# Kernel optimization log

Hardware: AMD Instinct MI355X
Metric: run time of the kernel (lower is better)

## Reference

```python
import jax, jax.numpy as jnp
import numpy as np

# Module constants (from init_kwargs)
NB_IN = 4          # num_blocks_in
NB_OUT = 8         # num_blocks_out
BS_IN = 128        # block_size_in (hard-coded in source)
NHID = 4096
BS_OUT = NHID // NB_OUT   # 512, also att_out
TOPK = 4
DK = 64            # d_k = d_v, n_head = 1


def _group_linear(x, w):
    # x: (B, n_blocks, d_in), w: (n_blocks, d_in, d_out) -> (B, n_blocks, d_out)
    return jnp.einsum('bnd,nde->bne', x, w)


def _attend(q, k, v):
    # single-head scaled dot-product attention
    attn = jax.nn.softmax(jnp.einsum('bqd,bkd->bqk', q, k) / jnp.sqrt(jnp.asarray(DK, q.dtype)), axis=-1)
    return jnp.einsum('bqk,bkd->bqd', attn, v), attn


def setup_inputs() -> dict:
    key = jax.random.key(0)
    ks = jax.random.split(key, 20)
    s = 0.02
    d = {
        'inp': jax.random.normal(ks[0], (1024, NB_IN * BS_IN), jnp.float32),
        'hx': jax.random.normal(ks[1], (1024, NHID), jnp.float32),
        'cx': jax.random.normal(ks[2], (1024, NHID), jnp.float32),
        # inp_att (residual=False): GroupLinear q/k/v + fc
        'ia_wq': jax.random.normal(ks[3], (NB_OUT, BS_OUT, DK), jnp.float32) * s,
        'ia_wk': jax.random.normal(ks[4], (NB_IN + 1, BS_IN, DK), jnp.float32) * s,
        'ia_wv': jax.random.normal(ks[5], (NB_IN + 1, BS_IN, DK), jnp.float32) * s,
        'ia_fc_w': jax.random.normal(ks[6], (DK, BS_OUT), jnp.float32) * s,
        'ia_fc_b': jnp.zeros((BS_OUT,), jnp.float32),
        # mha (residual=True, gated)
        'mha_wq': jax.random.normal(ks[7], (NB_OUT, BS_OUT, DK), jnp.float32) * s,
        'mha_wk': jax.random.normal(ks[8], (NB_OUT, BS_OUT, DK), jnp.float32) * s,
        'mha_wv': jax.random.normal(ks[9], (NB_OUT, BS_OUT, DK), jnp.float32) * s,
        'mha_fc_w': jax.random.normal(ks[10], (DK, BS_OUT), jnp.float32) * s,
        'mha_fc_b': jnp.zeros((BS_OUT,), jnp.float32),
        'mha_gate_w': jax.random.normal(ks[11], (DK, BS_OUT), jnp.float32) * s,
        'mha_gate_b': jnp.zeros((BS_OUT,), jnp.float32),
        # block-diagonal LSTM (BlockLSTM after blockify_params): per-block LSTMCell
        'w_ih': jax.random.normal(ks[12], (NB_OUT, BS_OUT, 4 * BS_OUT), jnp.float32) * s,
        'w_hh': jax.random.normal(ks[13], (NB_OUT, BS_OUT, 4 * BS_OUT), jnp.float32) * s,
        'b_ih': jnp.zeros((NB_OUT, 4 * BS_OUT), jnp.float32),
        'b_hh': jnp.zeros((NB_OUT, 4 * BS_OUT), jnp.float32),
    }
    return d


def _forward(inp, hx, cx, ia_wq, ia_wk, ia_wv, ia_fc_w, ia_fc_b,
             mha_wq, mha_wk, mha_wv, mha_fc_w, mha_fc_b, mha_gate_w, mha_gate_b,
             w_ih, w_hh, b_ih, b_hh):
    B = inp.shape[0]
    # --- input attention (inp_att) ---
    x = inp.reshape(B, NB_IN, BS_IN)
    x = jnp.concatenate([x, jnp.zeros_like(x[:, :1])], axis=1)        # append null block -> (B, NB_IN+1, BS_IN)
    hb = hx.reshape(B, NB_OUT, BS_OUT)
    q = _group_linear(hb, ia_wq)                                      # (B, NB_OUT, DK)
    k = _group_linear(x, ia_wk)
    v = _group_linear(x, ia_wv)
    o, iatt = _attend(q, k, v)                                        # o:(B,NB_OUT,DK), iatt:(B,NB_OUT,NB_IN+1)
    inp_use = (o @ ia_fc_w + ia_fc_b).reshape(B, NB_OUT * BS_OUT)     # residual=False path

    # --- top-k block selection mask (detached) ---
    score = iatt[:, :, 0]                                             # (B, NB_OUT)
    thr = jax.lax.top_k(score, TOPK)[0][:, -1]                        # k-th largest per sample
    mask_blk = (score > thr[:, None] - 0.01).astype(hx.dtype)         # (B, NB_OUT)
    mask = jnp.broadcast_to(mask_blk[:, :, None], (B, NB_OUT, BS_OUT)).reshape(B, NHID)
    mask = jax.lax.stop_gradient(mask)

    # --- block-diagonal LSTM update ---
    xb = inp_use.reshape(B, NB_OUT, BS_OUT)
    cb = cx.reshape(B, NB_OUT, BS_OUT)
    gates = (jnp.einsum('bkd,kdg->bkg', xb, w_ih) + b_ih
             + jnp.einsum('bkd,kdg->bkg', hb, w_hh) + b_hh)           # (B, NB_OUT, 4*BS_OUT)
    i_g, f_g, g_g, o_g = jnp.split(gates, 4, axis=-1)
    c_new = jax.nn.sigmoid(f_g) * cb + jax.nn.sigmoid(i_g) * jnp.tanh(g_g)
    h_new = jax.nn.sigmoid(o_g) * jnp.tanh(c_new)                     # (B, NB_OUT, BS_OUT)
    cx_new = c_new.reshape(B, NHID)

    # --- inter-block attention (step_att, residual + gate) ---
    residual = h_new
    q2 = _group_linear(h_new, mha_wq)
    k2 = _group_linear(h_new, mha_wk)
    v2 = _group_linear(h_new, mha_wv)
    o2, _ = _attend(q2, k2, v2)                                       # (B, NB_OUT, DK)
    out = o2 @ mha_fc_w + mha_fc_b
    gate = jax.nn.sigmoid(o2 @ mha_gate_w + mha_gate_b)
    hx_new = (residual + gate * jnp.tanh(out)).reshape(B, NHID)

    # --- masked blend of old / new states ---
    hx_out = mask * hx_new + (1.0 - mask) * hx
    cx_out = mask * cx_new + (1.0 - mask) * cx
    return hx_out, cx_out, mask


def reference(inp, hx, cx, ia_wq, ia_wk, ia_wv, ia_fc_w, ia_fc_b,
              mha_wq, mha_wk, mha_wv, mha_fc_w, mha_fc_b, mha_gate_w, mha_gate_b,
              w_ih, w_hh, b_ih, b_hh):
    return _forward(inp, hx, cx, ia_wq, ia_wk, ia_wv, ia_fc_w, ia_fc_b,
                    mha_wq, mha_wk, mha_wv, mha_fc_w, mha_fc_b, mha_gate_w, mha_gate_b,
                    w_ih, w_hh, b_ih, b_hh)
```

## Files before the change

kernel.cpp:

```cpp
#include <hip/hip_runtime.h>
#include <hip/hip_bf16.h>

#define B_    1024
#define NHID_ 4096
#define NBO   8
#define BSO   512
#define DK_   64

typedef __bf16 bf16;
typedef __bf16 bf16x2 __attribute__((ext_vector_type(2)));
typedef __bf16 bf16x4 __attribute__((ext_vector_type(4)));
typedef __bf16 bf16x8 __attribute__((ext_vector_type(8)));
typedef float  f32x4  __attribute__((ext_vector_type(4)));

__device__ __forceinline__ float sigf(float x){
    float e = __expf(-x);
    return __builtin_amdgcn_rcpf(1.0f + e);
}
__device__ __forceinline__ float ftanh(float x){
    float e = __expf(2.0f*x);
    return 1.0f - 2.0f*__builtin_amdgcn_rcpf(e + 1.0f);
}

__device__ __forceinline__ void gload16(const void* g, void* lds){
    __builtin_amdgcn_global_load_lds((const __attribute__((address_space(1))) unsigned int*)g,
                                     (__attribute__((address_space(3))) unsigned int*)lds,
                                     16, 0, 0);
}

__device__ __forceinline__ void sbar(){
    asm volatile("" ::: "memory");
    __builtin_amdgcn_s_barrier();
    asm volatile("" ::: "memory");
}
#define WAITVM(N) asm volatile("s_waitcnt vmcnt(" #N ")" ::: "memory")

__global__ __launch_bounds__(256) void k_prepqkv(
    const float* __restrict__ w_ih, const float* __restrict__ w_hh,
    const float* __restrict__ hx, const float* __restrict__ inp,
    const float* __restrict__ ia_wq, const float* __restrict__ ia_wk,
    const float* __restrict__ ia_wv,
    const float* __restrict__ mha_wq, const float* __restrict__ mha_wk,
    const float* __restrict__ mha_wv, const float* __restrict__ ia_fc_w,
    const float* __restrict__ fc_w, const float* __restrict__ gate_w,
    bf16* __restrict__ wT, bf16* __restrict__ hb16, bf16* __restrict__ wqkvT,
    bf16* __restrict__ iafcT, bf16* __restrict__ fcgT,
    float* __restrict__ qbufH, float* __restrict__ kbufH, float* __restrict__ vbufH)
{
    int bid = blockIdx.x;
    int t = threadIdx.x;
    __shared__ float Af[32][36];
    __shared__ float W1[32][68];
    __shared__ float W2[32][68];
    __shared__ float tile[64][65];

    if (bid < 768){
        int z = (bid >= 384) ? 1 : 0;
        int r = bid - z*384;
        int y = r >> 5, b0 = (r & 31)*32;
        int tx = t&15, ty = t>>4;
        if (y < 8){
            int n = y;
            float acc[2][4] = {};
            for (int k0=z*256; k0<z*256+256; k0+=32){
                { int row=t>>3, c4=(t&7)*4;
                  *(float4*)&Af[row][c4] = *(const float4*)&hx[(size_t)(b0+row)*4096 + n*512 + k0 + c4]; }
                #pragma unroll
                for (int j=0;j<2;++j){
                    int id = j*256 + t;
                    int kk = id>>4, e4 = (id&15)*4;
                    *(float4*)&W1[kk][e4] = *(const float4*)&ia_wq[(size_t)n*32768 + (size_t)(k0+kk)*64 + e4];
                }
                __syncthreads();
                #pragma unroll
                for (int kk4=0; kk4<8; ++kk4){
                    float4 a0 = *(float4*)&Af[ty*2  ][kk4*4];
                    float4 a1 = *(float4*)&Af[ty*2+1][kk4*4];
                    #pragma unroll
                    for (int j=0;j<4;++j){
                        float4 wv = *(float4*)&W1[kk4*4+j][tx*4];
                        float s0 = (j==0)?a0.x:((j==1)?a0.y:((j==2)?a0.z:a0.w));
                        float s1 = (j==0)?a1.x:((j==1)?a1.y:((j==2)?a1.z:a1.w));
                        acc[0][0]+=s0*wv.x; acc[0][1]+=s0*wv.y; acc[0][2]+=s0*wv.z; acc[0][3]+=s0*wv.w;
                        acc[1][0]+=s1*wv.x; acc[1][1]+=s1*wv.y; acc[1][2]+=s1*wv.z; acc[1][3]+=s1*wv.w;
                    }
                }
                __syncthreads();
            }
            #pragma unroll
            for (int r2=0;r2<2;++r2){
                float4 o; o.x=acc[r2][0]; o.y=acc[r2][1]; o.z=acc[r2][2]; o.w=acc[r2][3];
                *(float4*)&qbufH[((size_t)(z*B_ + b0+ty*2+r2))*512 + n*64 + tx*4] = o;
            }
        } else {
            int jb = y-8;
            float ak[2][4] = {}, av[2][4] = {};
            for (int k0=z*64; k0<z*64+64; k0+=32){
                { int row=t>>3, c4=(t&7)*4;
                  *(float4*)&Af[row][c4] = *(const float4*)&inp[(size_t)(b0+row)*512 + jb*128 + k0 + c4]; }
                #pragma unroll
                for (int j=0;j<2;++j){
                    int id = j*256 + t;
                    int kk = id>>4, e4 = (id&15)*4;
                    *(float4*)&W1[kk][e4] = *(const float4*)&ia_wk[(size_t)jb*8192 + (size_t)(k0+kk)*64 + e4];
                    *(float4*)&W2[kk][e4] = *(const float4*)&ia_wv[(size_t)jb*8192 + (size_t)(k0+kk)*64 + e4];
                }
                __syncthreads();
                #pragma unroll
                for (int kk4=0; kk4<8; ++kk4){
                    float4 a0 = *(float4*)&Af[ty*2  ][kk4*4];
                    float4 a1 = *(float4*)&Af[ty*2+1][kk4*4];
                    #pragma unroll
                    for (int j=0;j<4;++j){
                        float4 wk = *(float4*)&W1[kk4*4+j][tx*4];
                        float4 wv = *(float4*)&W2[kk4*4+j][tx*4];
                        float s0 = (j==0)?a0.x:((j==1)?a0.y:((j==2)?a0.z:a0.w));
                        float s1 = (j==0)?a1.x:((j==1)?a1.y:((j==2)?a1.z:a1.w));
                        ak[0][0]+=s0*wk.x; ak[0][1]+=s0*wk.y; ak[0][2]+=s0*wk.z; ak[0][3]+=s0*wk.w;
                        ak[1][0]+=s1*wk.x; ak[1][1]+=s1*wk.y; ak[1][2]+=s1*wk.z; ak[1][3]+=s1*wk.w;
                        av[0][0]+=s0*wv.x; av[0][1]+=s0*wv.y; av[0][2]+=s0*wv.z; av[0][3]+=s0*wv.w;
                        av[1][0]+=s1*wv.x; av[1][1]+=s1*wv.y; av[1][2]+=s1*wv.z; av[1][3]+=s1*wv.w;
                    }
                }
                __syncthreads();
            }
            #pragma unroll
            for (int r2=0;r2<2;++r2){
                float4 ok; ok.x=ak[r2][0]; ok.y=ak[r2][1]; ok.z=ak[r2][2]; ok.w=ak[r2][3];
                float4 ov; ov.x=av[r2][0]; ov.y=av[r2][1]; ov.z=av[r2][2]; ov.w=av[r2][3];
                *(float4*)&kbufH[((size_t)(z*B_ + b0+ty*2+r2))*256 + jb*64 + tx*4] = ok;
                *(float4*)&vbufH[((size_t)(z*B_ + b0+ty*2+r2))*256 + jb*64 + tx*4] = ov;
            }
        }
        return;
    }
    bid -= 768;
    if (bid < 4096){
        int c0 = (bid & 31)*64;
        int k0 = ((bid>>5)&7)*64;
        int z  = bid>>8;
        int n = z>>1, which = z&1;
        const float* src = (which ? w_hh : w_ih) + (size_t)n*512*2048;
        #pragma unroll
        for (int it=0; it<4; ++it){
            int idx = t + it*256;
            int r = idx>>4, c4 = (idx&15)*4;
            *(float4*)&tile[r][c4] = *(const float4*)&src[(size_t)(k0+r)*2048 + c0 + c4];
        }
        __syncthreads();
        #pragma unroll
        for (int it=0; it<2; ++it){
            int idx = t + it*256;
            int c = idx>>3, r8 = (idx&7)*8;
            bf16x8 v;
            #pragma unroll
            for (int jj=0;jj<8;++jj) v[jj] = (bf16)tile[r8+jj][c];
            *(bf16x8*)&wT[((size_t)n*2048 + c0 + c)*1024 + which*512 + k0 + r8] = v;
        }
        return;
    }
    int gid = (bid-4096)*256 + t;
    if (gid < 1048576){
        float4 v = ((const float4*)hx)[gid];
        bf16x4 o; o.x=(bf16)v.x; o.y=(bf16)v.y; o.z=(bf16)v.z; o.w=(bf16)v.w;
        *(bf16x4*)&hb16[(size_t)gid*4] = o;
        return;
    }
    int e = gid - 1048576;
    if (e < 786432){
        int col = e >> 9, k = e & 511;
        int n = col / 192, c = col - n*192;
        int p = c >> 6, ee = c & 63;
        const float* s = (p==0) ? mha_wq : ((p==1) ? mha_wk : mha_wv);
        wqkvT[e] = (bf16)s[((size_t)n*512 + k)*64 + ee];
        return;
    }
    e -= 786432;
    if (e < 32768){
        int c = e>>6, k = e&63;
        iafcT[e] = (bf16)ia_fc_w[(size_t)k*512 + c];
        return;
    }
    e -= 32768;
    if (e < 65536){
        int cg = e>>6, k = e&63;
        int ct = cg>>6, j = cg&63;
        const float* s = (j<32) ? fc_w : gate_w;
        int col = ct*32 + (j&31);
        fcgT[e] = (bf16)s[(size_t)k*512 + col];
    }
}

__global__ __launch_bounds__(512) void k_score(const float* __restrict__ qbufH,
                                               const float* __restrict__ kbufH,
                                               const float* __restrict__ vbufH,
                                               const bf16* __restrict__ iafcT,
                                               const float* __restrict__ ia_fc_b,
                                               bf16* __restrict__ xb16,
                                               float* __restrict__ maskb,
                                               float* __restrict__ mask_out)
{
    int t = threadIdx.x;
    int sb = t>>7, ts = t&127;
    int wv = (t>>6)&1, lw = t&63;
    int b = blockIdx.x*4 + sb;
    __shared__ float q_s[4][512];
    __shared__ float k_s[4][256];
    __shared__ float v_s[4][256];
    __shared__ float at_s[4][40];
    __shared__ float sc_s[4][8];
    __shared__ float mb_s[4][8];
    __shared__ bf16 o_s[32][72];

    #pragma unroll
    for (int r=0;r<4;++r){
        int i = ts + r*128;
        q_s[sb][i] = qbufH[(size_t)b*512 + i] + qbufH[(size_t)(B_+b)*512 + i];
    }
    #pragma unroll
    for (int r=0;r<2;++r){
        int i = ts + r*128;
        k_s[sb][i] = kbufH[(size_t)b*256 + i] + kbufH[(size_t)(B_+b)*256 + i];
        v_s[sb][i] = vbufH[(size_t)b*256 + i] + vbufH[(size_t)(B_+b)*256 + i];
    }
    __syncthreads();
    {
        int n = wv*4 + (lw>>4);
        int j = (lw>>2)&3;
        int ec = lw&3;
        const float* q = &q_s[sb][n*64 + ec*16];
        const float* k = &k_s[sb][j*64 + ec*16];
        float s = 0.f;
        #pragma unroll
        for (int e=0;e<16;++e) s += q[e]*k[e];
        s += __shfl_xor(s, 1);
        s += __shfl_xor(s, 2);
        if (ec==0) at_s[sb][n*5+j] = s*0.125f;
        if ((lw&15)==4) at_s[sb][n*5+4] = 0.f;
    }
    __syncthreads();
    if (lw < 4){
        int n = wv*4 + lw;
        float m = at_s[sb][n*5];
        for (int j=1;j<5;++j) m = fmaxf(m, at_s[sb][n*5+j]);
        float ex[5]; float sum=0.f;
        for (int j=0;j<5;++j){ ex[j]=__expf(at_s[sb][n*5+j]-m); sum+=ex[j]; }
        float inv = 1.f/sum;
        for (int j=0;j<5;++j) at_s[sb][n*5+j] = ex[j]*inv;
        sc_s[sb][n] = ex[0]*inv;
    }
    __syncthreads();
    if (ts == 0){
        float s[8];
        for (int nn=0;nn<8;++nn) s[nn] = sc_s[sb][nn];
        for (int ii=1;ii<8;++ii){ float key=s[ii]; int jj=ii-1;
            while(jj>=0 && s[jj]<key){ s[jj+1]=s[jj]; --jj; } s[jj+1]=key; }
        float thr = s[3]-0.01f;
        for (int nn=0;nn<8;++nn) mb_s[sb][nn] = (sc_s[sb][nn] > thr) ? 1.0f : 0.0f;
    }
    __syncthreads();
    #pragma unroll
    for (int r=0;r<4;++r){
        int i = ts + r*128;
        int n = i>>6, e = i&63;
        float s = 0.f;
        #pragma unroll
        for (int j=0;j<4;++j) s += at_s[sb][n*5+j]*v_s[sb][j*64+e];
        o_s[sb*8+n][e] = (bf16)s;
    }
    if (ts < 8) maskb[b*8+ts] = mb_s[sb][ts];
    float4* mo = (float4*)(mask_out + (size_t)b*4096);
    #pragma unroll
    for (int r=0;r<8;++r){
        int i4 = ts + r*128;
        float m = mb_s[sb][i4>>7];
        float4 mv; mv.x=m; mv.y=m; mv.z=m; mv.w=m;
        mo[i4] = mv;
    }
    __syncthreads();
    {
        int w = t>>6, l = t&63, quad = l>>4, l16 = l&15;
        int wm = w&1, wd = w>>1;
        bf16x8 a0 = *(const bf16x8*)&o_s[wm*16 + l16][quad*8];
        bf16x8 a1 = *(const bf16x8*)&o_s[wm*16 + l16][32 + quad*8];
        f32x4 zero = {0.f,0.f,0.f,0.f};
        #pragma unroll
        for (int nt=0; nt<8; ++nt){
            int cg = wd*128 + nt*16 + l16;
            bf16x8 b0 = *(const bf16x8*)&iafcT[(size_t)cg*64 + quad*8];
            bf16x8 b1 = *(const bf16x8*)&iafcT[(size_t)cg*64 + 32 + quad*8];
            f32x4 acc = __builtin_amdgcn_mfma_f32_16x16x32_bf16(a0, b0, zero, 0,0,0);
            acc = __builtin_amdgcn_mfma_f32_16x16x32_bf16(a1, b1, acc, 0,0,0);
            float bias = ia_fc_b[cg];
            #pragma unroll
            for (int v=0; v<4; ++v){
                int rm = wm*16 + quad*4 + v;
                int bb = blockIdx.x*4 + (rm>>3), nn = rm&7;
                xb16[(size_t)bb*4096 + nn*512 + cg] = (bf16)(acc[v] + bias);
            }
        }
    }
}

__global__ __launch_bounds__(512,2) void k_lstm(
    const bf16* __restrict__ xb16, const bf16* __restrict__ hb16,
    const bf16* __restrict__ wT, const float* __restrict__ b_ih,
    const float* __restrict__ b_hh, const float* __restrict__ cx,
    const float* __restrict__ maskb,
    float* __restrict__ cx_out, bf16* __restrict__ hn16)
{
    int bid = blockIdx.x;
    int n  = bid & 7;
    int i  = bid >> 3;
    int mt = i & 3, nt = i >> 2;
    int b0 = mt*256, d0 = nt*64;

    int t = threadIdx.x;
    int w = t >> 6, l = t & 63;
    int wr = w >> 2, wc = w & 3;
    int quad = l >> 4, l16 = l & 15;

    __shared__ __align__(16) bf16 lds[4*16384];

    int G0 = t;
    int rowA0 = G0>>2, rowA1 = rowA0 + 128;
    int ksA0 = (G0&3) ^ ((rowA0>>1)&3);
    int ksA1 = (G0&3) ^ ((rowA1>>1)&3);
    const bf16* xbP0 = xb16 + (size_t)(b0+rowA0)*4096 + n*512 + ksA0*8;
    const bf16* hbP0 = hb16 + (size_t)(b0+rowA0)*4096 + n*512 + ksA0*8;
    const bf16* xbP1 = xb16 + (size_t)(b0+rowA1)*4096 + n*512 + ksA1*8;
    const bf16* hbP1 = hb16 + (size_t)(b0+rowA1)*4096 + n*512 + ksA1*8;

    int vc0 = G0>>2, vc1 = vc0 + 128;
    int ksB0 = (G0&3) ^ ((vc0>>1)&3);
    int ksB1 = (G0&3) ^ ((vc1>>1)&3);
    const bf16* wb = wT + (size_t)n*2048*1024;
    const bf16* wP0 = wb + (size_t)((vc0>>6)*512 + d0 + (vc0&63))*1024 + ksB0*8;
    const bf16* wP1 = wb + (size_t)((vc1>>6)*512 + d0 + (vc1&63))*1024 + ksB1*8;

    int offA[8], offB[4];
    #pragma unroll
    for (int m=0;m<8;++m){ int R = wr*128 + m*16 + l16; offA[m] = (R*4 + (quad ^ ((R>>1)&3)))*8; }
    #pragma unroll
    for (int nf=0;nf<4;++nf){ int C = wc*64 + nf*16 + l16; offB[nf] = (C*4 + (quad ^ ((C>>1)&3)))*8; }

    auto stA = [&](int buf, int kt){
        const bf16* s0 = (kt<16 ? xbP0 : hbP0) + (kt&15)*32;
        const bf16* s1 = (kt<16 ? xbP1 : hbP1) + (kt&15)*32;
        bf16* dst = &lds[buf*16384 + w*512];
        gload16(s0, dst);
        gload16(s1, dst + 4096);
    };
    auto stB = [&](int buf, int kt){
        bf16* dst = &lds[buf*16384 + 8192 + w*512];
        gload16(wP0 + kt*32, dst);
        gload16(wP1 + kt*32, dst + 4096);
    };

    f32x4 zero = {0.f,0.f,0.f,0.f};
    f32x4 acc[8][4];
    #pragma unroll
    for (int m=0;m<8;++m)
        #pragma unroll
        for (int nf=0;nf<4;++nf) acc[m][nf] = zero;

    stA(0,0); stB(0,0);
    stA(1,1); stB(1,1);
    WAITVM(4);
    sbar();

    #pragma unroll 2
    for (int kt=0; kt<32; ++kt){
        int buf = kt & 3;
        const bf16* Ab = &lds[buf*16384];
        const bf16* Bb = Ab + 8192;

        if (kt < 30){ stA((kt+2)&3, kt+2); stB((kt+2)&3, kt+2); }

        bf16x8 av[8], bv[4];
        #pragma unroll
        for (int m=0;m<8;++m) av[m] = *(const bf16x8*)&Ab[offA[m]];
        #pragma unroll
        for (int nf=0;nf<4;++nf) bv[nf] = *(const bf16x8*)&Bb[offB[nf]];

        __builtin_amdgcn_s_setprio(1);
        #pragma unroll
        for (int m=0;m<8;++m)
            #pragma unroll
            for (int nf=0;nf<4;++nf)
                acc[m][nf] = __builtin_amdgcn_mfma_f32_16x16x32_bf16(av[m], bv[nf], acc[m][nf], 0,0,0);
        __builtin_amdgcn_s_setprio(0);

        if (kt < 30) { WAITVM(4); } else { WAITVM(0); }
        sbar();
    }

    float* gbuf = (float*)lds;
    const int GP = 260;
    int dl_t = t & 63;
    int i_t  = t >> 6;
    int d = d0 + dl_t;
    float bi  = b_ih[n*2048 +        d] + b_hh[n*2048 +        d];
    float bff = b_ih[n*2048 +  512 + d] + b_hh[n*2048 +  512 + d];
    float bg  = b_ih[n*2048 + 1024 + d] + b_hh[n*2048 + 1024 + d];
    float bo  = b_ih[n*2048 + 1536 + d] + b_hh[n*2048 + 1536 + d];

    #pragma unroll
    for (int c=0; c<4; ++c){
        if (wr == (c>>1)){
            #pragma unroll
            for (int mm=0; mm<4; ++mm)
                #pragma unroll
                for (int nf=0; nf<4; ++nf)
                    #pragma unroll
                    for (int v=0; v<4; ++v)
                        gbuf[(mm*16 + quad*4 + v)*GP + wc*64 + nf*16 + l16] = acc[(c&1)*4 + mm][nf][v];
        }
        __syncthreads();
        #pragma unroll
        for (int r=0; r<8; ++r){
            int row_l = i_t*8 + r;
            int row_g = b0 + c*64 + row_l;
            float gi = gbuf[row_l*GP +       dl_t] + bi;
            float gf = gbuf[row_l*GP +  64 + dl_t] + bff;
            float gg = gbuf[row_l*GP + 128 + dl_t] + bg;
            float go = gbuf[row_l*GP + 192 + dl_t] + bo;
            size_t gidx = (size_t)row_g*4096 + n*512 + d;
            float cb = cx[gidx];
            float cn = sigf(gf)*cb + sigf(gi)*ftanh(gg);
            float hn = sigf(go)*ftanh(cn);
            float mk = maskb[row_g*8 + n];
            cx_out[gidx] = (mk != 0.f) ? cn : cb;
            hn16[gidx]   = (bf16)hn;
        }
        __syncthreads();
    }
}

__global__ __launch_bounds__(256) void k_proj64(const bf16* __restrict__ hn16,
                                                const bf16* __restrict__ wqkvT,
                                                float* __restrict__ qkv2)
{
    int b0 = blockIdx.x*64, n = blockIdx.y, ct = blockIdx.z;
    int t = threadIdx.x, w = t>>6, l = t&63, quad = l>>4, l16 = l&15;
    int wm = w&1, wd = w>>1;
    __shared__ bf16 A_s[2][256*8];
    __shared__ bf16 B_s[2][256*8];
    f32x4 zero = {0.f,0.f,0.f,0.f};
    f32x4 acc[2][2] = {{zero,zero},{zero,zero}};
    const bf16* ab = hn16 + (size_t)n*512;
    const bf16* wb = wqkvT + ((size_t)n*192 + ct*64)*512;

    auto stage = [&](int buf, int k0){
        int row = t>>2, ss = t&3;
        int seg = ss ^ ((row>>1)&3);
        gload16(ab + (size_t)(b0+row)*4096 + k0 + seg*8, &A_s[buf][(w*64)*8]);
        gload16(wb + (size_t)row*512      + k0 + seg*8, &B_s[buf][(w*64)*8]);
    };

    stage(0, 0);
    for (int it=0; it<16; ++it){
        __syncthreads();
        if (it < 15) stage((it+1)&1, (it+1)*32);
        int buf = it&1;
        bf16x8 a[2], bb[2];
        #pragma unroll
        for (int r=0;r<2;++r){
            int row = wm*32 + r*16 + l16;
            int slot = row*4 + (quad ^ ((row>>1)&3));
            a[r] = *(const bf16x8*)&A_s[buf][slot*8];
        }
        #pragma unroll
        for (int c=0;c<2;++c){
            int col = wd*32 + c*16 + l16;
            int slot = col*4 + (quad ^ ((col>>1)&3));
            bb[c] = *(const bf16x8*)&B_s[buf][slot*8];
        }
        #pragma unroll
        for (int r=0;r<2;++r)
            #pragma unroll
            for (int c=0;c<2;++c)
                acc[r][c] = __builtin_amdgcn_mfma_f32_16x16x32_bf16(a[r], bb[c], acc[r][c], 0,0,0);
    }
    #pragma unroll
    for (int c=0;c<2;++c){
        int col = ct*64 + wd*32 + c*16 + l16;
        #pragma unroll
        for (int r=0;r<2;++r)
            #pragma unroll
            for (int v=0;v<4;++v){
                int row = b0 + wm*32 + r*16 + quad*4 + v;
                qkv2[(size_t)row*1536 + n*192 + col] = acc[r][c][v];
            }
    }
}

__global__ __launch_bounds__(512) void k_att2fc(const float* __restrict__ qkv2,
                                                const bf16* __restrict__ fcgT,
                                                const float* __restrict__ fc_b,
                                                const float* __restrict__ gate_b,
                                                const bf16* __restrict__ hn16,
                                                const float* __restrict__ hx,
                                                const float* __restrict__ maskb,
                                                float* __restrict__ hx_out)
{
    int t = threadIdx.x;
    int sb = t>>7, ts = t&127;
    int wv = (t>>6)&1, lw = t&63;
    int b = blockIdx.x*4 + sb;
    __shared__ float q_s[4][512];
    __shared__ float k_s[4][512];
    __shared__ float v_s[4][512];
    __shared__ float at_s[4][64];
    __shared__ bf16 o_s[32][72];
    #pragma unroll
    for (int r=0;r<4;++r){
        int i = ts + r*128;
        int n = i>>6, e = i&63;
        const float* src = qkv2 + (size_t)b*1536 + n*192;
        q_s[sb][i] = src[e];
        k_s[sb][i] = src[64+e];
        v_s[sb][i] = src[128+e];
    }
    __syncthreads();
    {
        int n = wv*4 + (lw>>4);
        int j = (lw>>1)&7;
        int eh = lw&1;
        const float* q = &q_s[sb][n*64 + eh*32];
        const float* k = &k_s[sb][j*64 + eh*32];
        float s = 0.f;
        #pragma unroll
        for (int e=0;e<32;++e) s += q[e]*k[e];
        s += __shfl_xor(s, 1);
        if (eh==0) at_s[sb][n*8+j] = s*0.125f;
    }
    __syncthreads();
    if (lw < 4){
        int n = wv*4 + lw;
        float m = at_s[sb][n*8];
        for (int j=1;j<8;++j) m = fmaxf(m, at_s[sb][n*8+j]);
        float ex[8]; float sum=0.f;
        for (int j=0;j<8;++j){ ex[j]=__expf(at_s[sb][n*8+j]-m); sum+=ex[j]; }
        float inv = 1.f/sum;
        for (int j=0;j<8;++j) at_s[sb][n*8+j] = ex[j]*inv;
    }
    __syncthreads();
    #pragma unroll
    for (int r=0;r<4;++r){
        int i = ts + r*128;
        int n = i>>6, e = i&63;
        float s = 0.f;
        #pragma unroll
        for (int j=0;j<8;++j) s += at_s[sb][n*8+j]*v_s[sb][j*64+e];
        o_s[sb*8+n][e] = (bf16)s;
    }
    __syncthreads();
    {
        int w = t>>6, l = t&63, quad = l>>4, l16 = l&15;
        int wm = w&1, wd = w>>1;
        bf16x8 a0 = *(const bf16x8*)&o_s[wm*16 + l16][quad*8];
        bf16x8 a1 = *(const bf16x8*)&o_s[wm*16 + l16][32 + quad*8];
        f32x4 zero = {0.f,0.f,0.f,0.f};
        f32x4 acc[16];
        #pragma unroll
        for (int nt=0; nt<16; ++nt){
            int cg = wd*256 + nt*16 + l16;
            bf16x8 b0 = *(const bf16x8*)&fcgT[(size_t)cg*64 + quad*8];
            bf16x8 b1 = *(const bf16x8*)&fcgT[(size_t)cg*64 + 32 + quad*8];
            acc[nt] = __builtin_amdgcn_mfma_f32_16x16x32_bf16(a0, b0, zero, 0,0,0);
            acc[nt] = __builtin_amdgcn_mfma_f32_16x16x32_bf16(a1, b1, acc[nt], 0,0,0);
        }
        #pragma unroll
        for (int ctl=0; ctl<4; ++ctl){
            int ct = wd*4 + ctl;
            #pragma unroll
            for (int s=0; s<2; ++s){
                int d = ct*32 + s*16 + l16;
                float fb = fc_b[d], gb = gate_b[d];
                f32x4 fa = acc[ctl*4+s], ga = acc[ctl*4+2+s];
                #pragma unroll
                for (int v=0; v<4; ++v){
                    int rm = wm*16 + quad*4 + v;
                    int bb = blockIdx.x*4 + (rm>>3), nn = rm&7;
                    size_t idx = (size_t)bb*4096 + nn*512 + d;
                    float f = fa[v] + fb;
                    float g = ga[v] + gb;
                    float hnv = (float)hn16[idx];
                    float mk = maskb[bb*8+nn];
                    hx_out[idx] = (mk != 0.f) ? (hnv + sigf(g)*ftanh(f)) : hx[idx];
                }
            }
        }
    }
}

extern "C" void kernel_launch(void* const* d_in, const int* in_sizes, int n_in,
                              void* d_out, int out_size, void* d_ws, size_t ws_size,
                              hipStream_t stream)
{
    const float* inp       = (const float*)d_in[0];
    const float* hx        = (const float*)d_in[1];
    const float* cx        = (const float*)d_in[2];
    const float* ia_wq     = (const float*)d_in[3];
    const float* ia_wk     = (const float*)d_in[4];
    const float* ia_wv     = (const float*)d_in[5];
    const float* ia_fc_w   = (const float*)d_in[6];
    const float* ia_fc_b   = (const float*)d_in[7];
    const float* mha_wq    = (const float*)d_in[8];
    const float* mha_wk    = (const float*)d_in[9];
    const float* mha_wv    = (const float*)d_in[10];
    const float* mha_fc_w  = (const float*)d_in[11];
    const float* mha_fc_b  = (const float*)d_in[12];
    const float* mha_gate_w= (const float*)d_in[13];
    const float* mha_gate_b= (const float*)d_in[14];
    const float* w_ih      = (const float*)d_in[15];
    const float* w_hh      = (const float*)d_in[16];
    const float* b_ih      = (const float*)d_in[17];
    const float* b_hh      = (const float*)d_in[18];

    float* hx_out  = (float*)d_out;
    float* cx_out  = hx_out + (size_t)B_*NHID_;
    float* mask_out= cx_out + (size_t)B_*NHID_;

    char* p = (char*)d_ws;
    bf16* wT     = (bf16*)p;               p += (size_t)8*2048*1024*2;
    bf16* hb16   = (bf16*)p;               p += (size_t)B_*NHID_*2;
    bf16* xb16   = (bf16*)p;               p += (size_t)B_*NHID_*2;
    bf16* hn16   = (bf16*)p;               p += (size_t)B_*NHID_*2;
    bf16* wqkvT  = (bf16*)p;               p += (size_t)8*192*512*2;
    bf16* iafcT  = (bf16*)p;               p += (size_t)512*64*2;
    bf16* fcgT   = (bf16*)p;               p += (size_t)1024*64*2;
    float* qbufH = (float*)p;              p += (size_t)2*B_*512*4;
    float* kbufH = (float*)p;              p += (size_t)2*B_*256*4;
    float* vbufH = (float*)p;              p += (size_t)2*B_*256*4;
    float* qkv2  = (float*)p;              p += (size_t)B_*1536*4;
    float* maskb = (float*)p;              p += (size_t)B_*8*4;

    hipLaunchKernelGGL(k_prepqkv, dim3(12416), dim3(256), 0, stream,
                       w_ih, w_hh, hx, inp, ia_wq, ia_wk, ia_wv,
                       mha_wq, mha_wk, mha_wv, ia_fc_w, mha_fc_w, mha_gate_w,
                       wT, hb16, wqkvT, iafcT, fcgT, qbufH, kbufH, vbufH);
    hipLaunchKernelGGL(k_score, dim3(256), dim3(512), 0, stream,
                       qbufH, kbufH, vbufH, iafcT, ia_fc_b, xb16, maskb, mask_out);
    hipLaunchKernelGGL(k_lstm, dim3(256), dim3(512), 0, stream,
                       xb16, hb16, wT, b_ih, b_hh, cx, maskb, cx_out, hn16);
    hipLaunchKernelGGL(k_proj64, dim3(16,8,3), dim3(256), 0, stream, hn16, wqkvT, qkv2);
    hipLaunchKernelGGL(k_att2fc, dim3(256), dim3(512), 0, stream,
                       qkv2, fcgT, mha_fc_b, mha_gate_b, hn16, hx, maskb, hx_out);
}
```

Baseline: 273.1 us.

## Tile weight transposes through LDS and triple-buffer k_proj64 loads

The small weight transposes in the prep kernel (mha q/k/v, ia_fc, fc/gate) move from one scalar strided access per element to tiles staged through shared memory, with coalesced float4 reads and bf16x8 writes. This cuts the prep grid size and avoids uncoalesced global traffic. The k_proj64 GEMM goes from a double-buffered to a triple-buffered async load pipeline with explicit vmcnt waits and raised priority around the MFMAs, so loads have more time to overlap compute. The cost is more shared memory per block and more complex synchronisation.

Result: no change. 273.5 us, median of 2 (+0.1%).

```diff
diff --git a/kernel.cpp b/kernel.cpp
--- a/kernel.cpp
+++ b/kernel.cpp
@@ -159,35 +159,79 @@
         }
         return;
     }
-    int gid = (bid-4096)*256 + t;
-    if (gid < 1048576){
+    bid -= 4096;
+    if (bid < 4096){
+        int gid = bid*256 + t;
         float4 v = ((const float4*)hx)[gid];
         bf16x4 o; o.x=(bf16)v.x; o.y=(bf16)v.y; o.z=(bf16)v.z; o.w=(bf16)v.w;
         *(bf16x4*)&hb16[(size_t)gid*4] = o;
         return;
     }
-    int e = gid - 1048576;
-    if (e < 786432){
-        int col = e >> 9, k = e & 511;
-        int n = col / 192, c = col - n*192;
-        int p = c >> 6, ee = c & 63;
+    bid -= 4096;
+    if (bid < 192){
+        int kt = bid & 7, np = bid >> 3;
+        int n = np / 3, p = np - n*3;
+        int k0 = kt*64;
         const float* s = (p==0) ? mha_wq : ((p==1) ? mha_wk : mha_wv);
-        wqkvT[e] = (bf16)s[((size_t)n*512 + k)*64 + ee];
+        #pragma unroll
+        for (int it=0; it<4; ++it){
+            int r = it*16 + (t>>4), c4 = (t&15)*4;
+            *(float4*)&tile[r][c4] = *(const float4*)&s[((size_t)n*512 + k0 + r)*64 + c4];
+        }
+        __syncthreads();
+        #pragma unroll
+        for (int it=0; it<2; ++it){
+            int idx = it*256 + t;
+            int ee = idx>>3, k8 = (idx&7)*8;
+            bf16x8 v;
+            #pragma unroll
+            for (int jj=0;jj<8;++jj) v[jj] = (bf16)tile[k8+jj][ee];
+            *(bf16x8*)&wqkvT[((size_t)n*192 + p*64 + ee)*512 + k0 + k8] = v;
+        }
         return;
     }
-    e -= 786432;
-    if (e < 32768){
-        int c = e>>6, k = e&63;
-        iafcT[e] = (bf16)ia_fc_w[(size_t)k*512 + c];
+    bid -= 192;
+    if (bid < 8){
+        int c0 = bid*64;
+        #pragma unroll
+        for (int it=0; it<4; ++it){
+            int k = it*16 + (t>>4), c4 = (t&15)*4;
+            *(float4*)&tile[k][c4] = *(const float4*)&ia_fc_w[(size_t)k*512 + c0 + c4];
+        }
+        __syncthreads();
+        #pragma unroll
+        for (int it=0; it<2; ++it){
+            int idx = it*256 + t;
+            int cc = idx>>3, k8 = (idx&7)*8;
+            bf16x8 v;
+            #pragma unroll
+            for (int jj=0;jj<8;++jj) v[jj] = (bf16)tile[k8+jj][cc];
+            *(bf16x8*)&iafcT[(size_t)(c0+cc)*64 + k8] = v;
+        }
         return;
     }
-    e -= 32768;
-    if (e < 65536){
-        int cg = e>>6, k = e&63;
-        int ct = cg>>6, j = cg&63;
-        const float* s = (j<32) ? fc_w : gate_w;
-        int col = ct*32 + (j&31);
-        fcgT[e] = (bf16)s[(size_t)k*512 + col];
+    bid -= 8;
+    if (bid < 16){
+        int ct = bid;
+        #pragma unroll
+        for (int it=0; it<4; ++it){
+            int k = it*16 + (t>>4);
+            int seg = t&15;
+            int j4 = seg*4;
+            const float* s = (seg < 8) ? &fc_w[(size_t)k*512 + ct*32 + j4]
+                                       : &gate_w[(size_t)k*512 + ct*32 + (j4-32)];
+            *(float4*)&tile[k][j4] = *(const float4*)s;
+        }
+        __syncthreads();
+        #pragma unroll
+        for (int it=0; it<2; ++it){
+            int idx = it*256 + t;
+            int j = idx>>3, k8 = (idx&7)*8;
+            bf16x8 v;
+            #pragma unroll
+            for (int jj=0;jj<8;++jj) v[jj] = (bf16)tile[k8+jj][j];
+            *(bf16x8*)&fcgT[(size_t)(ct*64 + j)*64 + k8] = v;
+        }
     }
 }
 
@@ -444,30 +488,38 @@
     int b0 = blockIdx.x*64, n = blockIdx.y, ct = blockIdx.z;
     int t = threadIdx.x, w = t>>6, l = t&63, quad = l>>4, l16 = l&15;
     int wm = w&1, wd = w>>1;
-    __shared__ bf16 A_s[2][256*8];
-    __shared__ bf16 B_s[2][256*8];
+    __shared__ __align__(16) bf16 A_s[3][256*8];
+    __shared__ __align__(16) bf16 B_s[3][256*8];
     f32x4 zero = {0.f,0.f,0.f,0.f};
     f32x4 acc[2][2] = {{zero,zero},{zero,zero}};
     const bf16* ab = hn16 + (size_t)n*512;
     const bf16* wb = wqkvT + ((size_t)n*192 + ct*64)*512;
 
-    auto stage = [&](int buf, int k0){
-        int row = t>>2, ss = t&3;
-        int seg = ss ^ ((row>>1)&3);
-        gload16(ab + (size_t)(b0+row)*4096 + k0 + seg*8, &A_s[buf][(w*64)*8]);
-        gload16(wb + (size_t)row*512      + k0 + seg*8, &B_s[buf][(w*64)*8]);
+    int row = t>>2, ss = t&3;
+    int seg = ss ^ ((row>>1)&3);
+    const bf16* aP = ab + (size_t)(b0+row)*4096 + seg*8;
+    const bf16* bP = wb + (size_t)row*512      + seg*8;
+
+    auto stage = [&](int buf, int kt){
+        gload16(aP + kt*32, &A_s[buf][(w*64)*8]);
+        gload16(bP + kt*32, &B_s[buf][(w*64)*8]);
     };
 
     stage(0, 0);
+    stage(1, 1);
+    WAITVM(2);
+    sbar();
+
+    int buf = 0;
+    #pragma unroll 1
     for (int it=0; it<16; ++it){
-        __syncthreads();
-        if (it < 15) stage((it+1)&1, (it+1)*32);
-        int buf = it&1;
+        int nb = (buf==0) ? 2 : buf-1;
+        if (it < 14) stage(nb, it+2);
         bf16x8 a[2], bb[2];
         #pragma unroll
         for (int r=0;r<2;++r){
-            int row = wm*32 + r*16 + l16;
-            int slot = row*4 + (quad ^ ((row>>1)&3));
+            int rr = wm*32 + r*16 + l16;
+            int slot = rr*4 + (quad ^ ((rr>>1)&3));
             a[r] = *(const bf16x8*)&A_s[buf][slot*8];
         }
         #pragma unroll
@@ -476,11 +528,16 @@
             int slot = col*4 + (quad ^ ((col>>1)&3));
             bb[c] = *(const bf16x8*)&B_s[buf][slot*8];
         }
+        __builtin_amdgcn_s_setprio(1);
         #pragma unroll
         for (int r=0;r<2;++r)
             #pragma unroll
             for (int c=0;c<2;++c)
                 acc[r][c] = __builtin_amdgcn_mfma_f32_16x16x32_bf16(a[r], bb[c], acc[r][c], 0,0,0);
+        __builtin_amdgcn_s_setprio(0);
+        if (it < 14) { WAITVM(2); } else { WAITVM(0); }
+        sbar();
+        buf = (buf==2) ? 0 : buf+1;
     }
     #pragma unroll
     for (int c=0;c<2;++c){
@@ -489,8 +546,8 @@
         for (int r=0;r<2;++r)
             #pragma unroll
             for (int v=0;v<4;++v){
-                int row = b0 + wm*32 + r*16 + quad*4 + v;
-                qkv2[(size_t)row*1536 + n*192 + col] = acc[r][c][v];
+                int rr = b0 + wm*32 + r*16 + quad*4 + v;
+                qkv2[(size_t)rr*1536 + n*192 + col] = acc[r][c][v];
             }
     }
 }
@@ -637,7 +694,7 @@
     float* qkv2  = (float*)p;              p += (size_t)B_*1536*4;
     float* maskb = (float*)p;              p += (size_t)B_*8*4;
 
-    hipLaunchKernelGGL(k_prepqkv, dim3(12416), dim3(256), 0, stream,
+    hipLaunchKernelGGL(k_prepqkv, dim3(9176), dim3(256), 0, stream,
                        w_ih, w_hh, hx, inp, ia_wq, ia_wk, ia_wv,
                        mha_wq, mha_wk, mha_wv, ia_fc_w, mha_fc_w, mha_gate_w,
                        wT, hb16, wqkvT, iafcT, fcgT, qbufH, kbufH, vbufH);
```
